# Performance work log

Hardware: AMD Instinct MI355X
Metric: run time of the kernel (lower is better)

Reference implementation:

```python
import jax, jax.numpy as jnp
import numpy as np

NUM_HEADS = 16

def setup_inputs() -> dict:
    key = jax.random.key(0)
    k_x, k_wq, k_bq, k_wo, k_bo = jax.random.split(key, 5)
    B, S, D = 4, 2048, 1024
    x = jax.random.normal(k_x, (B, S, D), dtype=jnp.float32)
    # Flax Dense default init: lecun_normal for kernel, zeros for bias; use small normals here.
    w_qkv = jax.random.normal(k_wq, (D, 3 * D), dtype=jnp.float32) * (D ** -0.5)
    b_qkv = jnp.zeros((3 * D,), dtype=jnp.float32)
    w_out = jax.random.normal(k_wo, (D, D), dtype=jnp.float32) * (D ** -0.5)
    b_out = jnp.zeros((D,), dtype=jnp.float32)
    return {"x": x, "w_qkv": w_qkv, "b_qkv": b_qkv, "w_out": w_out, "b_out": b_out}

def reference(x, w_qkv, b_qkv, w_out, b_out):
    B, S, D = x.shape
    H = NUM_HEADS
    hd = D // H
    scale = hd ** -0.5
    qkv = x @ w_qkv + b_qkv                                  # [B,S,3D]
    qkv = qkv.reshape(B, S, 3, H, hd)
    qkv = jnp.transpose(qkv, (2, 0, 3, 1, 4))                # [3,B,H,S,hd]
    q, k, v = qkv[0], qkv[1], qkv[2]
    attn = jnp.einsum("bhqd,bhkd->bhqk", q, k) * scale       # [B,H,S,S]
    attn = jax.nn.softmax(attn, axis=-1)
    out = jnp.einsum("bhqk,bhkd->bhqd", attn, v)             # [B,H,S,hd]
    out = jnp.transpose(out, (0, 2, 1, 3)).reshape(B, S, D)
    return out @ w_out + b_out
```

## Files before the change

kernel.cpp:

```cpp
#include <hip/hip_runtime.h>
#include <cstdint>
#include <cstddef>

#define B_    4
#define S_    2048
#define D_    1024
#define H_    16
#define HD_   64
#define M_    8192
#define NQKV  3072

typedef __bf16 bf16;
typedef __bf16 bf16x4 __attribute__((ext_vector_type(4)));
typedef __bf16 bf16x8 __attribute__((ext_vector_type(8)));
typedef float  f32x2  __attribute__((ext_vector_type(2)));
typedef float  f32x4  __attribute__((ext_vector_type(4)));
typedef float  f32x16 __attribute__((ext_vector_type(16)));
typedef unsigned short u16x4 __attribute__((ext_vector_type(4)));
typedef uint32_t u32x2 __attribute__((ext_vector_type(2)));
typedef uint32_t u32x4 __attribute__((ext_vector_type(4)));

__device__ __forceinline__ void gl2lds16(const void* g, void* l) {
  __builtin_amdgcn_global_load_lds(
      (__attribute__((address_space(1))) void*)(uintptr_t)g,
      (__attribute__((address_space(3))) void*)l, 16, 0, 0);
}

__device__ __forceinline__ uint32_t pkbf16(float a, float b) {
  union { bf16 h[2]; uint32_t u; } z;
  z.h[0] = (bf16)a; z.h[1] = (bf16)b;
  return z.u;
}

__global__ __launch_bounds__(256) void cast_f32_bf16(const float* __restrict__ in,
                                                     bf16* __restrict__ out, int n4) {
  int i = blockIdx.x * 256 + threadIdx.x;
  if (i >= n4) return;
  float4 v = ((const float4*)in)[i];
  bf16x4 o;
  o[0] = (bf16)v.x; o[1] = (bf16)v.y; o[2] = (bf16)v.z; o[3] = (bf16)v.w;
  ((bf16x4*)out)[i] = o;
}

__global__ __launch_bounds__(256) void transpose_cast(const float* __restrict__ in,
                                                      bf16* __restrict__ out, int R, int C) {
  __shared__ float tile[32][33];
  int bx = blockIdx.x * 32, by = blockIdx.y * 32;
  int tx = threadIdx.x, ty = threadIdx.y;
#pragma unroll
  for (int i = 0; i < 32; i += 8)
    tile[ty + i][tx] = in[(size_t)(by + ty + i) * C + bx + tx];
  __syncthreads();
#pragma unroll
  for (int i = 0; i < 32; i += 8)
    out[(size_t)(bx + ty + i) * R + by + tx] = (bf16)tile[tx][ty + i];
}

template <bool OUT_BF16>
__global__ __launch_bounds__(256) void gemm_bt(const bf16* __restrict__ A,
                                               const bf16* __restrict__ Bt,
                                               const float* __restrict__ bias,
                                               void* __restrict__ Cptr,
                                               int M, int N, int K) {
  __shared__ __align__(16) bf16 As[128 * 64];
  __shared__ __align__(16) bf16 Bs[128 * 64];
  const int tid  = threadIdx.x;
  const int lane = tid & 63, w = tid >> 6;
  const int lo   = lane & 15, quad = lane >> 4;
  const int xcd = blockIdx.x & 7, g = blockIdx.x >> 3;
  const int mi  = g & 7,          n = g >> 3;
  const int bm  = (xcd * 8 + mi) * 128, bn = n * 128;
  const int wm = (w >> 1) * 64,    wn = (w & 1) * 64;

  f32x4 acc[4][4];
  const f32x4 zero = {0.f, 0.f, 0.f, 0.f};
#pragma unroll
  for (int i = 0; i < 4; ++i)
#pragma unroll
    for (int j = 0; j < 4; ++j) acc[i][j] = zero;

  for (int k0 = 0; k0 < K; k0 += 64) {
#pragma unroll
    for (int c = 0; c < 4; ++c) {
      int seg = c * 4 + w;
      int idx = seg * 512 + lane * 8;
      int row = idx >> 6, col = idx & 63;
      gl2lds16(A  + (size_t)(bm + row) * K + k0 + col, As + seg * 512);
      gl2lds16(Bt + (size_t)(bn + row) * K + k0 + col, Bs + seg * 512);
    }
    __syncthreads();
#pragma unroll
    for (int ks = 0; ks < 2; ++ks) {
      bf16x8 av[4], bv[4];
#pragma unroll
      for (int i = 0; i < 4; ++i)
        av[i] = *(const bf16x8*)&As[(wm + i * 16 + lo) * 64 + ks * 32 + quad * 8];
#pragma unroll
      for (int j = 0; j < 4; ++j)
        bv[j] = *(const bf16x8*)&Bs[(wn + j * 16 + lo) * 64 + ks * 32 + quad * 8];
#pragma unroll
      for (int i = 0; i < 4; ++i)
#pragma unroll
        for (int j = 0; j < 4; ++j)
          acc[i][j] = __builtin_amdgcn_mfma_f32_16x16x32_bf16(av[i], bv[j], acc[i][j], 0, 0, 0);
    }
    __syncthreads();
  }
#pragma unroll
  for (int j = 0; j < 4; ++j) {
    int cg = bn + wn + j * 16 + lo;
    float bsv = bias[cg];
#pragma unroll
    for (int i = 0; i < 4; ++i) {
      int rg = bm + wm + i * 16 + quad * 4;
#pragma unroll
      for (int r = 0; r < 4; ++r) {
        float v = acc[i][j][r] + bsv;
        if (OUT_BF16) ((bf16*)Cptr)[(size_t)(rg + r) * N + cg] = (bf16)v;
        else          ((float*)Cptr)[(size_t)(rg + r) * N + cg] = v;
      }
    }
  }
}

__global__ __launch_bounds__(256, 2) void gemm_bt_wide(const bf16* __restrict__ A,
                                                       const bf16* __restrict__ Bt,
                                                       const float* __restrict__ bias,
                                                       bf16* __restrict__ Cptr,
                                                       int M, int N, int K) {
  __shared__ __align__(16) bf16 As[128 * 64];
  __shared__ __align__(16) bf16 Bs[256 * 64];
  const int tid  = threadIdx.x;
  const int lane = tid & 63, w = tid >> 6;
  const int lo   = lane & 15, quad = lane >> 4;
  const int xcd = blockIdx.x & 7, g = blockIdx.x >> 3;
  const int mi  = g & 7,          n = g >> 3;
  const int bm  = (xcd * 8 + mi) * 128, bn = n * 256;
  const int wm = (w >> 1) * 64,    wn = (w & 1) * 128;

  f32x4 acc[4][8];
  const f32x4 zero = {0.f, 0.f, 0.f, 0.f};
#pragma unroll
  for (int i = 0; i < 4; ++i)
#pragma unroll
    for (int j = 0; j < 8; ++j) acc[i][j] = zero;

  for (int k0 = 0; k0 < K; k0 += 64) {
#pragma unroll
    for (int c = 0; c < 4; ++c) {
      int seg = c * 4 + w;
      int idx = seg * 512 + lane * 8;
      int row = idx >> 6, col = idx & 63;
      gl2lds16(A + (size_t)(bm + row) * K + k0 + col, As + seg * 512);
    }
#pragma unroll
    for (int c = 0; c < 8; ++c) {
      int seg = c * 4 + w;
      int idx = seg * 512 + lane * 8;
      int row = idx >> 6, col = idx & 63;
      gl2lds16(Bt + (size_t)(bn + row) * K + k0 + col, Bs + seg * 512);
    }
    __syncthreads();
#pragma unroll
    for (int ks = 0; ks < 2; ++ks) {
      bf16x8 av[4], bv[8];
#pragma unroll
      for (int i = 0; i < 4; ++i)
        av[i] = *(const bf16x8*)&As[(wm + i * 16 + lo) * 64 + ks * 32 + quad * 8];
#pragma unroll
      for (int j = 0; j < 8; ++j)
        bv[j] = *(const bf16x8*)&Bs[(wn + j * 16 + lo) * 64 + ks * 32 + quad * 8];
#pragma unroll
      for (int i = 0; i < 4; ++i)
#pragma unroll
        for (int j = 0; j < 8; ++j)
          acc[i][j] = __builtin_amdgcn_mfma_f32_16x16x32_bf16(av[i], bv[j], acc[i][j], 0, 0, 0);
    }
    __syncthreads();
  }
#pragma unroll
  for (int j = 0; j < 8; ++j) {
    int cg = bn + wn + j * 16 + lo;
    float bsv = bias[cg];
#pragma unroll
    for (int i = 0; i < 4; ++i) {
      int rg = bm + wm + i * 16 + quad * 4;
#pragma unroll
      for (int r = 0; r < 4; ++r)
        Cptr[(size_t)(rg + r) * N + cg] = (bf16)(acc[i][j][r] + bsv);
    }
  }
}

__global__ __launch_bounds__(256, 4) void flash_attn(const bf16* __restrict__ qkv,
                                                     bf16* __restrict__ out) {
  __shared__ __align__(16) bf16 Ks[2][64 * 64];
  __shared__ __align__(16) bf16 Vs[2][64 * 64];

  const int tid  = threadIdx.x;
  const int lane = tid & 63, wq = tid >> 6;
  const int l31  = lane & 31;
  const int e    = lane >> 5;
  const int hi8  = e * 8, hi4 = e * 4;

  const int bid = blockIdx.x;
  const int qb  = bid >> 6;
  const int bh  = bid & 63;
  const int h   = bh & 15;
  const int b   = bh >> 4;
  const int q0  = qb * 128;
  const size_t rowb = (size_t)b * S_;
  const bf16* qbase = qkv + rowb * NQKV + h * HD_;
  const bf16* kbase = qbase + D_;
  const bf16* vbase = qbase + 2 * D_;

  bf16x8 qf[4];
  {
    const bf16* qrow = qbase + (size_t)(q0 + wq * 32 + l31) * NQKV;
#pragma unroll
    for (int c = 0; c < 4; ++c)
      qf[c] = *(const bf16x8*)(qrow + c * 16 + hi8);
  }

  int kq_off[2];
#pragma unroll
  for (int it = 0; it < 2; ++it) {
    int ci = it * 256 + tid;
    int s  = ci >> 3;
    int x  = (ci & 7) ^ (s & 7);
    kq_off[it] = s * NQKV + x * 8;
  }
  int vs_d[2], vs_s[2], vs_off[2];
#pragma unroll
  for (int u = 0; u < 2; ++u) {
    int idx = u * 256 + tid;
    int d0 = (idx & 31) * 2;
    int s0 = (idx >> 5) * 4;
    vs_d[u] = d0;
    vs_s[u] = s0;
    vs_off[u] = (((s0 >> 3) ^ ((d0 >> 1) & 7)) * 8) + (s0 & 7);
  }

  uint32_t vreg[2][4];

#pragma unroll
  for (int it = 0; it < 2; ++it)
    gl2lds16(kbase + kq_off[it], &Ks[0][(it * 256 + wq * 64) * 8]);
#pragma unroll
  for (int u = 0; u < 2; ++u)
#pragma unroll
    for (int j = 0; j < 4; ++j)
      vreg[u][j] = *(const uint32_t*)(vbase + (size_t)(vs_s[u] + j) * NQKV + vs_d[u]);

  const f32x16 zero16 = {0.f,0.f,0.f,0.f,0.f,0.f,0.f,0.f,0.f,0.f,0.f,0.f,0.f,0.f,0.f,0.f};
  f32x16 oacc[2];
  oacc[0] = zero16; oacc[1] = zero16;
  f32x2 psv = {0.f, 0.f};
  const float c2 = 0.125f * 1.44269504088896341f;

  for (int kt = 0; kt < 32; ++kt) {
    const int buf = kt & 1;
#pragma unroll
    for (int u = 0; u < 2; ++u) {
      int d0 = vs_d[u];
      uint32_t lo0 = __builtin_amdgcn_perm(vreg[u][1], vreg[u][0], 0x05040100u);
      uint32_t lo1 = __builtin_amdgcn_perm(vreg[u][3], vreg[u][2], 0x05040100u);
      uint32_t hi0 = __builtin_amdgcn_perm(vreg[u][1], vreg[u][0], 0x07060302u);
      uint32_t hi1 = __builtin_amdgcn_perm(vreg[u][3], vreg[u][2], 0x07060302u);
      u32x2 lov = {lo0, lo1}, hiv = {hi0, hi1};
      *(u32x2*)&Vs[buf][(d0 + 0) * 64 + vs_off[u]] = lov;
      *(u32x2*)&Vs[buf][(d0 + 1) * 64 + vs_off[u]] = hiv;
    }
    __syncthreads();

    {
      int ktn = (kt + 1 < 32) ? kt + 1 : 31;
      const bf16* kb = kbase + (size_t)ktn * 64 * NQKV;
#pragma unroll
      for (int it = 0; it < 2; ++it)
        gl2lds16(kb + kq_off[it], &Ks[buf ^ 1][(it * 256 + wq * 64) * 8]);
    }
    {
      int ktn = (kt + 1 < 32) ? kt + 1 : 31;
      const bf16* vb = vbase + (size_t)ktn * 64 * NQKV;
#pragma unroll
      for (int u = 0; u < 2; ++u)
#pragma unroll
        for (int j = 0; j < 4; ++j)
          vreg[u][j] = *(const uint32_t*)(vb + (size_t)(vs_s[u] + j) * NQKV + vs_d[u]);
    }

    f32x16 sacc[2];
#pragma unroll
    for (int kk = 0; kk < 2; ++kk) {
      sacc[kk] = zero16;
      int srow = kk * 32 + l31;
      int swz  = (srow & 7) * 8;
#pragma unroll
      for (int c = 0; c < 4; ++c) {
        bf16x8 kf = *(const bf16x8*)&Ks[buf][srow * 64 + ((c * 16 + hi8) ^ swz)];
        sacc[kk] = __builtin_amdgcn_mfma_f32_32x32x16_bf16(kf, qf[c], sacc[kk], 0, 0, 0);
      }
    }

#pragma unroll
    for (int kk = 0; kk < 2; ++kk) {
      uint32_t Q8[8];
#pragma unroll
      for (int i = 0; i < 8; ++i) {
        f32x2 sv;
        sv[0] = sacc[kk][2 * i];
        sv[1] = sacc[kk][2 * i + 1];
        f32x2 t = sv * c2 - 16.0f;
        float p0 = __builtin_amdgcn_exp2f(t[0]);
        float p1 = __builtin_amdgcn_exp2f(t[1]);
        psv += (f32x2){p0, p1};
        Q8[i] = pkbf16(p0, p1);
      }
#pragma unroll
      for (int mh = 0; mh < 2; ++mh) {
        const int m = kk * 2 + mh, bq = mh * 4;
        u32x4 pd;
#if __has_builtin(__builtin_amdgcn_permlane32_swap)
        u32x2 w0 = __builtin_amdgcn_permlane32_swap(Q8[bq],     Q8[bq + 2], false, false);
        u32x2 w1 = __builtin_amdgcn_permlane32_swap(Q8[bq + 1], Q8[bq + 3], false, false);
        pd[0] = w0[0]; pd[1] = w1[0]; pd[2] = w0[1]; pd[3] = w1[1];
#else
        uint32_t s0 = e ? Q8[bq]     : Q8[bq + 2];
        uint32_t s1 = e ? Q8[bq + 1] : Q8[bq + 3];
        uint32_t r0 = __shfl_xor(s0, 32);
        uint32_t r1 = __shfl_xor(s1, 32);
        pd[0] = e ? r0 : Q8[bq];
        pd[1] = e ? r1 : Q8[bq + 1];
        pd[2] = e ? Q8[bq + 2] : r0;
        pd[3] = e ? Q8[bq + 3] : r1;
#endif
        bf16x8 pf = __builtin_bit_cast(bf16x8, pd);
#pragma unroll
        for (int dt = 0; dt < 2; ++dt) {
          int drow = dt * 32 + l31;
          int swv  = (drow >> 1) & 7;
          bf16x8 vf = *(const bf16x8*)&Vs[buf][drow * 64 + (((m * 2 + e) ^ swv) * 8)];
          oacc[dt] = __builtin_amdgcn_mfma_f32_32x32x16_bf16(vf, pf, oacc[dt], 0, 0, 0);
        }
      }
    }
  }

  float lsum = psv[0] + psv[1];
  lsum += __shfl_xor(lsum, 32);

  __syncthreads();
  bf16* Os = (bf16*)Vs;
  {
    float inv = 1.f / lsum;
    int ql = wq * 32 + l31;
    int swO = (ql >> 1) & 7;
#pragma unroll
    for (int dt = 0; dt < 2; ++dt) {
#pragma unroll
      for (int g = 0; g < 4; ++g) {
        bf16x4 ov;
#pragma unroll
        for (int jj = 0; jj < 4; ++jj) ov[jj] = (bf16)(oacc[dt][g * 4 + jj] * inv);
        *(bf16x4*)&Os[ql * 64 + (((dt * 4 + g) ^ swO) * 8) + hi4] = ov;
      }
    }
  }
  __syncthreads();
#pragma unroll
  for (int it = 0; it < 4; ++it) {
    int idx = it * 256 + tid;
    int row = idx >> 3, c8 = idx & 7;
    bf16x8 t = *(const bf16x8*)&Os[row * 64 + ((c8 ^ ((row >> 1) & 7)) * 8)];
    *(bf16x8*)&out[(rowb + q0 + row) * D_ + h * HD_ + c8 * 8] = t;
  }
}

extern "C" void kernel_launch(void* const* d_in, const int* in_sizes, int n_in,
                              void* d_out, int out_size, void* d_ws, size_t ws_size,
                              hipStream_t stream) {
  const float* x     = (const float*)d_in[0];
  const float* w_qkv = (const float*)d_in[1];
  const float* b_qkv = (const float*)d_in[2];
  const float* w_out = (const float*)d_in[3];
  const float* b_out = (const float*)d_in[4];
  float* out = (float*)d_out;

  char* ws = (char*)d_ws;
  bf16* xb    = (bf16*)(ws);
  bf16* wqkvT = (bf16*)(ws + (size_t)16777216);
  bf16* woutT = (bf16*)(ws + (size_t)23068672);
  bf16* qkvb  = (bf16*)(ws + (size_t)25165824);
  bf16* attnb = (bf16*)(ws + (size_t)75497472);

  cast_f32_bf16<<<(M_ * D_ / 4 + 255) / 256, 256, 0, stream>>>(x, xb, M_ * D_ / 4);
  transpose_cast<<<dim3(NQKV / 32, D_ / 32), dim3(32, 8), 0, stream>>>(w_qkv, wqkvT, D_, NQKV);
  transpose_cast<<<dim3(D_ / 32, D_ / 32), dim3(32, 8), 0, stream>>>(w_out, woutT, D_, D_);

  gemm_bt_wide<<<(M_ / 128) * (NQKV / 256), 256, 0, stream>>>(
      xb, wqkvT, b_qkv, qkvb, M_, NQKV, D_);

  flash_attn<<<B_ * H_ * (S_ / 128), 256, 0, stream>>>(qkvb, attnb);

  gemm_bt<false><<<(M_ / 128) * (D_ / 128), 256, 0, stream>>>(
      attnb, woutT, b_out, (void*)out, M_, D_, D_);
}
```

Baseline: 294.6 us.

## Deepen K/V prefetch pipeline in attention loop and add MFMA priority hints

Restructures the attention key loop into a two-step unrolled software pipeline. The K tile is DMA'd one step ahead, V registers are loaded two steps ahead in alternating register sets, and V is transposed into LDS after compute, with explicit waitcnt plus a raw barrier replacing __syncthreads. It also raises wave priority around the MFMA blocks. The aim is to hide global load latency behind matrix compute and cut barrier stalls, at the cost of more registers and fragile hand-tuned vmcnt counts.

```diff
diff --git a/kernel.cpp b/kernel.cpp
--- a/kernel.cpp
+++ b/kernel.cpp
@@ -241,16 +241,7 @@
     vs_off[u] = (((s0 >> 3) ^ ((d0 >> 1) & 7)) * 8) + (s0 & 7);
   }
 
-  uint32_t vreg[2][4];
-
-#pragma unroll
-  for (int it = 0; it < 2; ++it)
-    gl2lds16(kbase + kq_off[it], &Ks[0][(it * 256 + wq * 64) * 8]);
-#pragma unroll
-  for (int u = 0; u < 2; ++u)
-#pragma unroll
-    for (int j = 0; j < 4; ++j)
-      vreg[u][j] = *(const uint32_t*)(vbase + (size_t)(vs_s[u] + j) * NQKV + vs_d[u]);
+  uint32_t vE[2][4], vO[2][4];
 
   const f32x16 zero16 = {0.f,0.f,0.f,0.f,0.f,0.f,0.f,0.f,0.f,0.f,0.f,0.f,0.f,0.f,0.f,0.f};
   f32x16 oacc[2];
@@ -258,39 +249,37 @@
   f32x2 psv = {0.f, 0.f};
   const float c2 = 0.125f * 1.44269504088896341f;
 
-  for (int kt = 0; kt < 32; ++kt) {
-    const int buf = kt & 1;
-#pragma unroll
-    for (int u = 0; u < 2; ++u) {
-      int d0 = vs_d[u];
-      uint32_t lo0 = __builtin_amdgcn_perm(vreg[u][1], vreg[u][0], 0x05040100u);
-      uint32_t lo1 = __builtin_amdgcn_perm(vreg[u][3], vreg[u][2], 0x05040100u);
-      uint32_t hi0 = __builtin_amdgcn_perm(vreg[u][1], vreg[u][0], 0x07060302u);
-      uint32_t hi1 = __builtin_amdgcn_perm(vreg[u][3], vreg[u][2], 0x07060302u);
-      u32x2 lov = {lo0, lo1}, hiv = {hi0, hi1};
-      *(u32x2*)&Vs[buf][(d0 + 0) * 64 + vs_off[u]] = lov;
-      *(u32x2*)&Vs[buf][(d0 + 1) * 64 + vs_off[u]] = hiv;
-    }
-    __syncthreads();
-
-    {
-      int ktn = (kt + 1 < 32) ? kt + 1 : 31;
-      const bf16* kb = kbase + (size_t)ktn * 64 * NQKV;
-#pragma unroll
-      for (int it = 0; it < 2; ++it)
-        gl2lds16(kb + kq_off[it], &Ks[buf ^ 1][(it * 256 + wq * 64) * 8]);
-    }
-    {
-      int ktn = (kt + 1 < 32) ? kt + 1 : 31;
-      const bf16* vb = vbase + (size_t)ktn * 64 * NQKV;
-#pragma unroll
-      for (int u = 0; u < 2; ++u)
-#pragma unroll
-        for (int j = 0; j < 4; ++j)
-          vreg[u][j] = *(const uint32_t*)(vb + (size_t)(vs_s[u] + j) * NQKV + vs_d[u]);
-    }
-
+#define KDMA(KT, PB) {                                                      \
+    const bf16* kb_ = kbase + (size_t)(KT) * 64 * NQKV;                     \
+    _Pragma("unroll")                                                       \
+    for (int it = 0; it < 2; ++it)                                          \
+      gl2lds16(kb_ + kq_off[it], &Ks[PB][(it * 256 + wq * 64) * 8]);        \
+  }
+#define VLOAD(KT, VR) {                                                     \
+    const bf16* vb_ = vbase + (size_t)(KT) * 64 * NQKV;                     \
+    _Pragma("unroll")                                                       \
+    for (int u = 0; u < 2; ++u)                                             \
+      _Pragma("unroll")                                                     \
+      for (int j = 0; j < 4; ++j)                                           \
+        VR[u][j] = *(const uint32_t*)(vb_ + (size_t)(vs_s[u] + j) * NQKV + vs_d[u]); \
+  }
+#define VWRITE(VR, PB) {                                                    \
+    _Pragma("unroll")                                                       \
+    for (int u = 0; u < 2; ++u) {                                           \
+      int d0_ = vs_d[u];                                                    \
+      uint32_t lo0 = __builtin_amdgcn_perm(VR[u][1], VR[u][0], 0x05040100u);\
+      uint32_t lo1 = __builtin_amdgcn_perm(VR[u][3], VR[u][2], 0x05040100u);\
+      uint32_t hi0 = __builtin_amdgcn_perm(VR[u][1], VR[u][0], 0x07060302u);\
+      uint32_t hi1 = __builtin_amdgcn_perm(VR[u][3], VR[u][2], 0x07060302u);\
+      u32x2 lov = {lo0, lo1}, hiv = {hi0, hi1};                             \
+      *(u32x2*)&Vs[PB][(d0_ + 0) * 64 + vs_off[u]] = lov;                   \
+      *(u32x2*)&Vs[PB][(d0_ + 1) * 64 + vs_off[u]] = hiv;                   \
+    }                                                                       \
+  }
+
+  auto compute = [&](int P) __attribute__((always_inline)) {
     f32x16 sacc[2];
+    __builtin_amdgcn_s_setprio(1);
 #pragma unroll
     for (int kk = 0; kk < 2; ++kk) {
       sacc[kk] = zero16;
@@ -298,11 +287,11 @@
       int swz  = (srow & 7) * 8;
 #pragma unroll
       for (int c = 0; c < 4; ++c) {
-        bf16x8 kf = *(const bf16x8*)&Ks[buf][srow * 64 + ((c * 16 + hi8) ^ swz)];
+        bf16x8 kf = *(const bf16x8*)&Ks[P][srow * 64 + ((c * 16 + hi8) ^ swz)];
         sacc[kk] = __builtin_amdgcn_mfma_f32_32x32x16_bf16(kf, qf[c], sacc[kk], 0, 0, 0);
       }
     }
-
+    __builtin_amdgcn_s_setprio(0);
 #pragma unroll
     for (int kk = 0; kk < 2; ++kk) {
       uint32_t Q8[8];
@@ -336,16 +325,45 @@
         pd[3] = e ? Q8[bq + 3] : r1;
 #endif
         bf16x8 pf = __builtin_bit_cast(bf16x8, pd);
+        __builtin_amdgcn_s_setprio(1);
 #pragma unroll
         for (int dt = 0; dt < 2; ++dt) {
           int drow = dt * 32 + l31;
           int swv  = (drow >> 1) & 7;
-          bf16x8 vf = *(const bf16x8*)&Vs[buf][drow * 64 + (((m * 2 + e) ^ swv) * 8)];
+          bf16x8 vf = *(const bf16x8*)&Vs[P][drow * 64 + (((m * 2 + e) ^ swv) * 8)];
           oacc[dt] = __builtin_amdgcn_mfma_f32_32x32x16_bf16(vf, pf, oacc[dt], 0, 0, 0);
         }
+        __builtin_amdgcn_s_setprio(0);
       }
     }
-  }
+  };
+
+#define BODY(KT, P, VWR, VLD) {                                             \
+    int kn1 = (KT) + 1 < 32 ? (KT) + 1 : 31;                                \
+    int kn2 = (KT) + 2 < 32 ? (KT) + 2 : 31;                                \
+    KDMA(kn1, (P) ^ 1);                           \
+    VLOAD(kn2, VLD);               \
+    compute(P);                                                             \
+    VWRITE(VWR, (P) ^ 1);                  \
+    asm volatile("s_waitcnt vmcnt(8) lgkmcnt(0)" ::: "memory");             \
+    __builtin_amdgcn_s_barrier();                                           \
+  }
+
+  KDMA(0, 0);
+  VLOAD(0, vE);
+  VLOAD(1, vO);
+  VWRITE(vE, 0);
+  asm volatile("s_waitcnt vmcnt(8) lgkmcnt(0)" ::: "memory");
+  __builtin_amdgcn_s_barrier();
+
+  for (int t = 0; t < 16; ++t) {
+    BODY(2 * t,     0, vO, vE);
+    BODY(2 * t + 1, 1, vE, vO);
+  }
+#undef BODY
+#undef VWRITE
+#undef VLOAD
+#undef KDMA
 
   float lsum = psv[0] + psv[1];
   lsum += __shfl_xor(lsum, 32);
```

Result: slower. 412.3 us (+40.0%).

## Process two 32-row query tiles per wave in flash attention

Applied to the files above, without the earlier changes.

Each wave now handles 64 query rows instead of 32, so the attention block covers 256 queries and each K/V tile loaded into LDS is reused across twice as many MFMAs. This halves the grid size and the total K/V global traffic and LDS staging per query. In exchange it doubles the accumulator and score registers per wave, lowers the launch-bounds occupancy hint from 4 to 2, and leaves only 512 blocks, which may fill the device less evenly.

```diff
diff --git a/kernel.cpp b/kernel.cpp
--- a/kernel.cpp
+++ b/kernel.cpp
@@ -192,10 +192,11 @@
   }
 }
 
-__global__ __launch_bounds__(256, 4) void flash_attn(const bf16* __restrict__ qkv,
+__global__ __launch_bounds__(256, 2) void flash_attn(const bf16* __restrict__ qkv,
                                                      bf16* __restrict__ out) {
-  __shared__ __align__(16) bf16 Ks[2][64 * 64];
-  __shared__ __align__(16) bf16 Vs[2][64 * 64];
+  __shared__ __align__(16) bf16 smem[16384];
+  bf16* const Ksm = smem;
+  bf16* const Vsm = smem + 8192;
 
   const int tid  = threadIdx.x;
   const int lane = tid & 63, wq = tid >> 6;
@@ -208,18 +209,21 @@
   const int bh  = bid & 63;
   const int h   = bh & 15;
   const int b   = bh >> 4;
-  const int q0  = qb * 128;
+  const int q0  = qb * 256;
   const size_t rowb = (size_t)b * S_;
   const bf16* qbase = qkv + rowb * NQKV + h * HD_;
   const bf16* kbase = qbase + D_;
   const bf16* vbase = qbase + 2 * D_;
 
-  bf16x8 qf[4];
+  bf16x8 qfA[4], qfB[4];
   {
-    const bf16* qrow = qbase + (size_t)(q0 + wq * 32 + l31) * NQKV;
-#pragma unroll
-    for (int c = 0; c < 4; ++c)
-      qf[c] = *(const bf16x8*)(qrow + c * 16 + hi8);
+    const bf16* qrow0 = qbase + (size_t)(q0 + wq * 64 + l31) * NQKV;
+    const bf16* qrow1 = qrow0 + (size_t)32 * NQKV;
+#pragma unroll
+    for (int c = 0; c < 4; ++c) {
+      qfA[c] = *(const bf16x8*)(qrow0 + c * 16 + hi8);
+      qfB[c] = *(const bf16x8*)(qrow1 + c * 16 + hi8);
+    }
   }
 
   int kq_off[2];
@@ -245,7 +249,7 @@
 
 #pragma unroll
   for (int it = 0; it < 2; ++it)
-    gl2lds16(kbase + kq_off[it], &Ks[0][(it * 256 + wq * 64) * 8]);
+    gl2lds16(kbase + kq_off[it], Ksm + (it * 256 + wq * 64) * 8);
 #pragma unroll
   for (int u = 0; u < 2; ++u)
 #pragma unroll
@@ -253,9 +257,10 @@
       vreg[u][j] = *(const uint32_t*)(vbase + (size_t)(vs_s[u] + j) * NQKV + vs_d[u]);
 
   const f32x16 zero16 = {0.f,0.f,0.f,0.f,0.f,0.f,0.f,0.f,0.f,0.f,0.f,0.f,0.f,0.f,0.f,0.f};
-  f32x16 oacc[2];
-  oacc[0] = zero16; oacc[1] = zero16;
-  f32x2 psv = {0.f, 0.f};
+  f32x16 oacc[2][2];
+  oacc[0][0] = zero16; oacc[0][1] = zero16;
+  oacc[1][0] = zero16; oacc[1][1] = zero16;
+  f32x2 psA = {0.f, 0.f}, psB = {0.f, 0.f};
   const float c2 = 0.125f * 1.44269504088896341f;
 
   for (int kt = 0; kt < 32; ++kt) {
@@ -268,8 +273,8 @@
       uint32_t hi0 = __builtin_amdgcn_perm(vreg[u][1], vreg[u][0], 0x07060302u);
       uint32_t hi1 = __builtin_amdgcn_perm(vreg[u][3], vreg[u][2], 0x07060302u);
       u32x2 lov = {lo0, lo1}, hiv = {hi0, hi1};
-      *(u32x2*)&Vs[buf][(d0 + 0) * 64 + vs_off[u]] = lov;
-      *(u32x2*)&Vs[buf][(d0 + 1) * 64 + vs_off[u]] = hiv;
+      *(u32x2*)&Vsm[buf * 4096 + (d0 + 0) * 64 + vs_off[u]] = lov;
+      *(u32x2*)&Vsm[buf * 4096 + (d0 + 1) * 64 + vs_off[u]] = hiv;
     }
     __syncthreads();
 
@@ -278,7 +283,7 @@
       const bf16* kb = kbase + (size_t)ktn * 64 * NQKV;
 #pragma unroll
       for (int it = 0; it < 2; ++it)
-        gl2lds16(kb + kq_off[it], &Ks[buf ^ 1][(it * 256 + wq * 64) * 8]);
+        gl2lds16(kb + kq_off[it], Ksm + (buf ^ 1) * 4096 + (it * 256 + wq * 64) * 8);
     }
     {
       int ktn = (kt + 1 < 32) ? kt + 1 : 31;
@@ -290,86 +295,114 @@
           vreg[u][j] = *(const uint32_t*)(vb + (size_t)(vs_s[u] + j) * NQKV + vs_d[u]);
     }
 
-    f32x16 sacc[2];
 #pragma unroll
     for (int kk = 0; kk < 2; ++kk) {
-      sacc[kk] = zero16;
+      f32x16 sA = zero16, sB = zero16;
       int srow = kk * 32 + l31;
       int swz  = (srow & 7) * 8;
 #pragma unroll
       for (int c = 0; c < 4; ++c) {
-        bf16x8 kf = *(const bf16x8*)&Ks[buf][srow * 64 + ((c * 16 + hi8) ^ swz)];
-        sacc[kk] = __builtin_amdgcn_mfma_f32_32x32x16_bf16(kf, qf[c], sacc[kk], 0, 0, 0);
+        bf16x8 kf = *(const bf16x8*)&Ksm[buf * 4096 + srow * 64 + ((c * 16 + hi8) ^ swz)];
+        sA = __builtin_amdgcn_mfma_f32_32x32x16_bf16(kf, qfA[c], sA, 0, 0, 0);
+        sB = __builtin_amdgcn_mfma_f32_32x32x16_bf16(kf, qfB[c], sB, 0, 0, 0);
       }
-    }
-
-#pragma unroll
-    for (int kk = 0; kk < 2; ++kk) {
-      uint32_t Q8[8];
+
+      uint32_t Q8a[8], Q8b[8];
 #pragma unroll
       for (int i = 0; i < 8; ++i) {
-        f32x2 sv;
-        sv[0] = sacc[kk][2 * i];
-        sv[1] = sacc[kk][2 * i + 1];
-        f32x2 t = sv * c2 - 16.0f;
-        float p0 = __builtin_amdgcn_exp2f(t[0]);
-        float p1 = __builtin_amdgcn_exp2f(t[1]);
-        psv += (f32x2){p0, p1};
-        Q8[i] = pkbf16(p0, p1);
+        f32x2 sva, svb;
+        sva[0] = sA[2 * i]; sva[1] = sA[2 * i + 1];
+        svb[0] = sB[2 * i]; svb[1] = sB[2 * i + 1];
+        f32x2 ta = sva * c2 - 16.0f;
+        f32x2 tb = svb * c2 - 16.0f;
+        float a0 = __builtin_amdgcn_exp2f(ta[0]);
+        float a1 = __builtin_amdgcn_exp2f(ta[1]);
+        float b0 = __builtin_amdgcn_exp2f(tb[0]);
+        float b1 = __builtin_amdgcn_exp2f(tb[1]);
+        psA += (f32x2){a0, a1};
+        psB += (f32x2){b0, b1};
+        Q8a[i] = pkbf16(a0, a1);
+        Q8b[i] = pkbf16(b0, b1);
       }
+
 #pragma unroll
       for (int mh = 0; mh < 2; ++mh) {
         const int m = kk * 2 + mh, bq = mh * 4;
-        u32x4 pd;
+        u32x4 pda, pdb;
 #if __has_builtin(__builtin_amdgcn_permlane32_swap)
-        u32x2 w0 = __builtin_amdgcn_permlane32_swap(Q8[bq],     Q8[bq + 2], false, false);
-        u32x2 w1 = __builtin_amdgcn_permlane32_swap(Q8[bq + 1], Q8[bq + 3], false, false);
-        pd[0] = w0[0]; pd[1] = w1[0]; pd[2] = w0[1]; pd[3] = w1[1];
+        u32x2 wa0 = __builtin_amdgcn_permlane32_swap(Q8a[bq],     Q8a[bq + 2], false, false);
+        u32x2 wa1 = __builtin_amdgcn_permlane32_swap(Q8a[bq + 1], Q8a[bq + 3], false, false);
+        pda[0] = wa0[0]; pda[1] = wa1[0]; pda[2] = wa0[1]; pda[3] = wa1[1];
+        u32x2 wb0 = __builtin_amdgcn_permlane32_swap(Q8b[bq],     Q8b[bq + 2], false, false);
+        u32x2 wb1 = __builtin_amdgcn_permlane32_swap(Q8b[bq + 1], Q8b[bq + 3], false, false);
+        pdb[0] = wb0[0]; pdb[1] = wb1[0]; pdb[2] = wb0[1]; pdb[3] = wb1[1];
 #else
-        uint32_t s0 = e ? Q8[bq]     : Q8[bq + 2];
-        uint32_t s1 = e ? Q8[bq + 1] : Q8[bq + 3];
-        uint32_t r0 = __shfl_xor(s0, 32);
-        uint32_t r1 = __shfl_xor(s1, 32);
-        pd[0] = e ? r0 : Q8[bq];
-        pd[1] = e ? r1 : Q8[bq + 1];
-        pd[2] = e ? Q8[bq + 2] : r0;
-        pd[3] = e ? Q8[bq + 3] : r1;
+        {
+          uint32_t s0 = e ? Q8a[bq]     : Q8a[bq + 2];
+          uint32_t s1 = e ? Q8a[bq + 1] : Q8a[bq + 3];
+          uint32_t r0 = __shfl_xor(s0, 32);
+          uint32_t r1 = __shfl_xor(s1, 32);
+          pda[0] = e ? r0 : Q8a[bq];
+          pda[1] = e ? r1 : Q8a[bq + 1];
+          pda[2] = e ? Q8a[bq + 2] : r0;
+          pda[3] = e ? Q8a[bq + 3] : r1;
+        }
+        {
+          uint32_t s0 = e ? Q8b[bq]     : Q8b[bq + 2];
+          uint32_t s1 = e ? Q8b[bq + 1] : Q8b[bq + 3];
+          uint32_t r0 = __shfl_xor(s0, 32);
+          uint32_t r1 = __shfl_xor(s1, 32);
+          pdb[0] = e ? r0 : Q8b[bq];
+          pdb[1] = e ? r1 : Q8b[bq + 1];
+          pdb[2] = e ? Q8b[bq + 2] : r0;
+          pdb[3] = e ? Q8b[bq + 3] : r1;
+        }
 #endif
-        bf16x8 pf = __builtin_bit_cast(bf16x8, pd);
+        bf16x8 pfa = __builtin_bit_cast(bf16x8, pda);
+        bf16x8 pfb = __builtin_bit_cast(bf16x8, pdb);
 #pragma unroll
         for (int dt = 0; dt < 2; ++dt) {
           int drow = dt * 32 + l31;
           int swv  = (drow >> 1) & 7;
-          bf16x8 vf = *(const bf16x8*)&Vs[buf][drow * 64 + (((m * 2 + e) ^ swv) * 8)];
-          oacc[dt] = __builtin_amdgcn_mfma_f32_32x32x16_bf16(vf, pf, oacc[dt], 0, 0, 0);
+          bf16x8 vf = *(const bf16x8*)&Vsm[buf * 4096 + drow * 64 + (((m * 2 + e) ^ swv) * 8)];
+          oacc[dt][0] = __builtin_amdgcn_mfma_f32_32x32x16_bf16(vf, pfa, oacc[dt][0], 0, 0, 0);
+          oacc[dt][1] = __builtin_amdgcn_mfma_f32_32x32x16_bf16(vf, pfb, oacc[dt][1], 0, 0, 0);
         }
       }
     }
   }
 
-  float lsum = psv[0] + psv[1];
-  lsum += __shfl_xor(lsum, 32);
+  float lsumA = psA[0] + psA[1];
+  float lsumB = psB[0] + psB[1];
+  lsumA += __shfl_xor(lsumA, 32);
+  lsumB += __shfl_xor(lsumB, 32);
 
   __syncthreads();
-  bf16* Os = (bf16*)Vs;
+  bf16* Os = smem;
   {
-    float inv = 1.f / lsum;
-    int ql = wq * 32 + l31;
-    int swO = (ql >> 1) & 7;
-#pragma unroll
-    for (int dt = 0; dt < 2; ++dt) {
-#pragma unroll
-      for (int g = 0; g < 4; ++g) {
-        bf16x4 ov;
-#pragma unroll
-        for (int jj = 0; jj < 4; ++jj) ov[jj] = (bf16)(oacc[dt][g * 4 + jj] * inv);
-        *(bf16x4*)&Os[ql * 64 + (((dt * 4 + g) ^ swO) * 8) + hi4] = ov;
+    float invA = 1.f / lsumA;
+    float invB = 1.f / lsumB;
+#pragma unroll
+    for (int qs = 0; qs < 2; ++qs) {
+      float inv = qs ? invB : invA;
+      int ql = wq * 64 + qs * 32 + l31;
+      int swO = (ql >> 1) & 7;
+#pragma unroll
+      for (int dt = 0; dt < 2; ++dt) {
+#pragma unroll
+        for (int g = 0; g < 4; ++g) {
+          bf16x4 ov;
+#pragma unroll
+          for (int jj = 0; jj < 4; ++jj)
+            ov[jj] = (bf16)(oacc[dt][qs][g * 4 + jj] * inv);
+          *(bf16x4*)&Os[ql * 64 + (((dt * 4 + g) ^ swO) * 8) + hi4] = ov;
+        }
       }
     }
   }
   __syncthreads();
 #pragma unroll
-  for (int it = 0; it < 4; ++it) {
+  for (int it = 0; it < 8; ++it) {
     int idx = it * 256 + tid;
     int row = idx >> 3, c8 = idx & 7;
     bf16x8 t = *(const bf16x8*)&Os[row * 64 + ((c8 ^ ((row >> 1) & 7)) * 8)];
@@ -401,7 +434,7 @@
   gemm_bt_wide<<<(M_ / 128) * (NQKV / 256), 256, 0, stream>>>(
       xb, wqkvT, b_qkv, qkvb, M_, NQKV, D_);
 
-  flash_attn<<<B_ * H_ * (S_ / 128), 256, 0, stream>>>(qkvb, attnb);
+  flash_attn<<<B_ * H_ * (S_ / 256), 256, 0, stream>>>(qkvb, attnb);
 
   gemm_bt<false><<<(M_ / 128) * (D_ / 128), 256, 0, stream>>>(
       attnb, woutT, b_out, (void*)out, M_, D_, D_);
```

Measured after the change: 283.2 us. 3.9% less time.
